# Kernel tuning notes

Hardware: AMD Instinct MI355X
Metric: run time of the kernel (lower is better)

## Reference

```python
import jax, jax.numpy as jnp
import numpy as np

XBOUND = (-30.0, 30.0, 0.25)
YBOUND = (-15.0, 15.0, 0.25)
ZBOUND = (-1.0, 1.0, 0.5)
EPS = 1e-9


def _heights():
    n = int((ZBOUND[1] - ZBOUND[0]) // ZBOUND[2]) + 1
    return [ZBOUND[0] + i * ZBOUND[2] for i in range(n)]


def _bev_planes():
    # matches construct_plane_grid: linspace endpoints included, meshgrid(y, x) 'ij'
    num_x = int((XBOUND[1] - XBOUND[0]) / XBOUND[2])
    num_y = int((YBOUND[1] - YBOUND[0]) / YBOUND[2])
    x = jnp.linspace(XBOUND[0], XBOUND[1], num_x, dtype=jnp.float32)
    y = jnp.linspace(YBOUND[0], YBOUND[1], num_y, dtype=jnp.float32)
    yy, xx = jnp.meshgrid(y, x, indexing='ij')
    planes = [jnp.stack([xx, yy, jnp.full_like(xx, h)], axis=-1) for h in _heights()]
    return jnp.stack(planes)  # (nlvl, bH, bW, 3)


def _bilinear_grid_sample(im, grid):
    # faithful port of the manual pad+floor+gather grid_sample (align_corners=False)
    n, c, h, w = im.shape
    gh, gw = grid.shape[1], grid.shape[2]
    x = ((grid[..., 0] + 1) * w - 1) / 2
    y = ((grid[..., 1] + 1) * h - 1) / 2
    x = x.reshape(n, -1)
    y = y.reshape(n, -1)
    x0 = jnp.floor(x)
    y0 = jnp.floor(y)
    wa = ((x0 + 1 - x) * (y0 + 1 - y))[:, None, :]
    wb = ((x0 + 1 - x) * (y - y0))[:, None, :]
    wc = ((x - x0) * (y0 + 1 - y))[:, None, :]
    wd = ((x - x0) * (y - y0))[:, None, :]
    pw, ph = w + 2, h + 2
    # clip in float first to avoid int32 overflow; out-of-range lands on zero padding either way
    x0f = jnp.clip(x0, -2.0, w + 2.0)
    y0f = jnp.clip(y0, -2.0, h + 2.0)
    x0i = jnp.clip(x0f.astype(jnp.int32) + 1, 0, pw - 1)
    x1i = jnp.clip(x0f.astype(jnp.int32) + 2, 0, pw - 1)
    y0i = jnp.clip(y0f.astype(jnp.int32) + 1, 0, ph - 1)
    y1i = jnp.clip(y0f.astype(jnp.int32) + 2, 0, ph - 1)
    im_flat = jnp.pad(im, ((0, 0), (0, 0), (1, 1), (1, 1))).reshape(n, c, -1)

    def gather(xi, yi):
        return jnp.take_along_axis(im_flat, (xi + yi * pw)[:, None, :], axis=2)

    out = (gather(x0i, y0i) * wa + gather(x0i, y1i) * wb
           + gather(x1i, y0i) * wc + gather(x1i, y1i) * wd)
    return out.reshape(n, c, gh, gw)


def _campos(pts, ego2cam, img_h, img_w):
    # pts: (B, q, 3); ego2cam: (B, ncam, 4, 4)
    B, q, _ = pts.shape
    ncam = ego2cam.shape[1]
    pts_h = jnp.concatenate([pts, jnp.ones_like(pts[..., :1])], axis=-1)  # (B,q,4)
    cam = jnp.einsum('bnij,bqj->bnqi', ego2cam, pts_h)  # (B,ncam,q,4)
    z = cam[..., 2:3]
    mask = z > EPS
    xy = cam[..., 0:2] / z + EPS
    px = xy[..., 0:1] / img_w
    py = xy[..., 1:2] / img_h
    p = (jnp.concatenate([px, py], axis=-1) - 0.5) * 2
    mask = (mask & (p[..., 0:1] > -1.0) & (p[..., 0:1] < 1.0)
            & (p[..., 1:2] > -1.0) & (p[..., 1:2] < 1.0))
    return p.reshape(B * ncam, q, 2), mask.reshape(B, ncam, q)


def reference(cam_feat, ego2cam, conv_w, conv_b, img_h, img_w):
    B, ncam = ego2cam.shape[0], ego2cam.shape[1]
    C = cam_feat.shape[1]
    planes = _bev_planes().astype(cam_feat.dtype)  # (nlvl,bH,bW,3)
    nlvl, bH, bW, _ = planes.shape
    pts = jnp.broadcast_to(planes.reshape(1, -1, 3), (B, nlvl * bH * bW, 3))
    pos, mask = _campos(pts, ego2cam, img_h, img_w)
    grid = pos.reshape(B * ncam, nlvl * bH, bW, 2)
    proj = _bilinear_grid_sample(cam_feat, grid).reshape(B, ncam, C, nlvl, bH, bW)
    m = mask.reshape(B, ncam, 1, nlvl, bH, bW).astype(proj.dtype)
    feat = (proj * m).sum(axis=1)            # (B,C,nlvl,bH,bW)
    num = m.sum(axis=1)                      # (B,1,nlvl,bH,bW)
    feat = feat / jnp.where(num == 0, jnp.ones_like(num), num)
    coords = jnp.broadcast_to(jnp.transpose(planes, (3, 0, 1, 2))[None], (B, 3, nlvl, bH, bW))
    feat = jnp.concatenate([feat, coords], axis=1).reshape(B, (C + 3) * nlvl, bH, bW)
    out = jax.lax.conv_general_dilated(
        feat, conv_w, window_strides=(1, 1), padding=((1, 1), (1, 1)),
        dimension_numbers=('NCHW', 'OIHW', 'NCHW'))
    return out + conv_b[None, :, None, None]


def setup_inputs() -> dict:
    key = jax.random.key(0)
    k1, k2, k3 = jax.random.split(key, 3)
    B, ncam, C = 1, 6, 128
    cH, cW = 64, 176
    nlvl = 5
    cam_feat = jax.random.normal(k1, (B * ncam, C, cH, cW), dtype=jnp.float32)
    ego2cam = jax.random.normal(k2, (B, ncam, 4, 4), dtype=jnp.float32)
    conv_w = jax.random.normal(k3, (128, (C + 3) * nlvl, 3, 3), dtype=jnp.float32) * 0.02
    conv_b = jnp.zeros((128,), dtype=jnp.float32)
    return {'cam_feat': cam_feat, 'ego2cam': ego2cam, 'conv_w': conv_w,
            'conv_b': conv_b, 'img_h': 512, 'img_w': 1408}
```

## Files before the change

kernel.cpp:

```cpp
#include <hip/hip_runtime.h>
#include <hip/hip_bf16.h>

#define BH 120
#define BW 240
#define NLVL 5
#define NCAM 6
#define CH 128
#define FH 64
#define FW 176
#define CIN 655
#define CINP 672
#define NCT 21
#define FROWS 124
#define FCOLS 242
#define NPIX (BH*BW)

typedef __hip_bfloat16 bf16;
typedef __attribute__((ext_vector_type(8))) short s16x8;
typedef __attribute__((ext_vector_type(4))) float f32x4;
typedef __attribute__((ext_vector_type(2))) float f32x2;
typedef unsigned int uint;
typedef __attribute__((ext_vector_type(4), aligned(4))) uint uint4a;

#define G_AS __attribute__((address_space(1)))
#define L_AS __attribute__((address_space(3)))

__device__ __forceinline__ float bf2f(unsigned short u) {
    union { unsigned int i; float f; } c; c.i = ((unsigned int)u) << 16; return c.f;
}
__device__ __forceinline__ uint f2bu(float x) {
    return (uint)__hip_bfloat16_raw(__float2bfloat16(x)).x;
}

__global__ __launch_bounds__(256) void transpose_kernel(
    const float* __restrict__ in, float* __restrict__ out)
{
    __shared__ float t[32][129];
    int n = blockIdx.z, h = blockIdx.y, w0 = blockIdx.x * 32;
    int wlim = min(32, FW - w0);
    int wx = threadIdx.x & 31, cg = threadIdx.x >> 5;
    if (wx < wlim) {
        #pragma unroll
        for (int k = 0; k < 16; ++k) {
            int c = cg + k * 8;
            t[wx][c] = in[((n*CH + c)*FH + h)*FW + w0 + wx];
        }
    }
    __syncthreads();
    int c2 = threadIdx.x & 127, wi = threadIdx.x >> 7;
    for (int w = wi; w < wlim; w += 2)
        out[((n*FH + h)*FW + w0 + w)*CH + c2] = t[w][c2];
}

__global__ __launch_bounds__(256) void wprep_kernel(
    const float* __restrict__ w, bf16* __restrict__ wbf)
{
    int idx = blockIdx.x * 256 + threadIdx.x;
    if (idx >= 128 * CINP) return;
    int oc = idx / CINP, cin = idx - oc * CINP;
    float v[9];
    if (cin < CIN) {
        const float* s = w + ((size_t)oc * CIN + cin) * 9;
        #pragma unroll
        for (int k = 0; k < 9; ++k) v[k] = s[k];
    } else {
        #pragma unroll
        for (int k = 0; k < 9; ++k) v[k] = 0.f;
    }
    #pragma unroll
    for (int k = 0; k < 9; ++k)
        wbf[(size_t)(k * 128 + oc) * CINP + cin] = __float2bfloat16(v[k]);
}

__global__ __launch_bounds__(128) void border_kernel(bf16* __restrict__ feat)
{
    int b = blockIdx.x;
    int row, col;
    if (b < 242)      { row = 0;   col = b; }
    else if (b < 484) { row = 121; col = b - 242; }
    else if (b < 604) { row = b - 484 + 1; col = 0; }
    else              { row = b - 604 + 1; col = 241; }
    s16x8* p = (s16x8*)(feat + ((size_t)row*FCOLS + col)*CINP);
    int t = threadIdx.x;
    if (t < 84) p[t] = (s16x8){0,0,0,0,0,0,0,0};
}

__global__ __launch_bounds__(256) void proj_kernel(
    const float* __restrict__ camt,
    const float* __restrict__ e2c,
    const int* __restrict__ pimgh, const int* __restrict__ pimgw,
    bf16* __restrict__ feat)
{
    __shared__ int   s_soff[4][32];
    __shared__ float s_w4[4][30][4];
    __shared__ int   s_val[4][32];

    const int wv = threadIdx.x >> 6;
    const int lane = threadIdx.x & 63;
    const int pix = blockIdx.x * 4 + wv;
    const int bx = pix % BW, by = pix / BW;
    float xw = (float)(-30.0 + bx * (60.0/239.0)); if (bx == BW-1) xw = 30.f;
    float yw = (float)(-15.0 + by * (30.0/119.0)); if (by == BH-1) yw = 15.f;

    const bool act = lane < 30;
    int valid = 0, ix = 0, iy = 0, cam = 0;
    float fx = 0.f, fy = 0.f;
    if (act) {
        int l = lane / 6; cam = lane - l*6;
        float h = -1.f + 0.5f * (float)l;
        const float* M = e2c + cam * 16;
        float cx = M[0]*xw + M[1]*yw + M[2]*h  + M[3];
        float cy = M[4]*xw + M[5]*yw + M[6]*h  + M[7];
        float cz = M[8]*xw + M[9]*yw + M[10]*h + M[11];
        float iw = (float)pimgw[0], ih = (float)pimgh[0];
        float px = ((cx/cz + 1e-9f)/iw - 0.5f) * 2.f;
        float py = ((cy/cz + 1e-9f)/ih - 0.5f) * 2.f;
        valid = (cz > 1e-9f) && (px > -1.f) && (px < 1.f)
                             && (py > -1.f) && (py < 1.f);
        float xs = ((px + 1.f)*(float)FW - 1.f) * 0.5f;
        float ys = ((py + 1.f)*(float)FH - 1.f) * 0.5f;
        float x0 = floorf(xs), y0 = floorf(ys);
        fx = xs - x0; fy = ys - y0;
        ix = (int)x0; iy = (int)y0;
        s_val[wv][lane] = valid;
    }
    __syncthreads();
    if (act) {
        int lbase = (lane / 6) * 6;
        int cnt = s_val[wv][lbase] + s_val[wv][lbase+1] + s_val[wv][lbase+2]
                + s_val[wv][lbase+3] + s_val[wv][lbase+4] + s_val[wv][lbase+5];
        float inv = (cnt > 0) ? (1.f / (float)cnt) : 0.f;
        float sc = valid ? inv : 0.f;
        int bx0 = min(max(ix, 0), FW-2);
        int by0 = min(max(iy, 0), FH-2);
        float gx0 = (1.f - fx) * sc, gx1 = fx * sc;
        float wx0 = 0.f, wx1 = 0.f;
        if (ix >= 0)     { if (ix == bx0) wx0 += gx0; else wx1 += gx0; }
        if (ix+1 <= FW-1){ if (ix+1 == bx0) wx0 += gx1; else wx1 += gx1; }
        float wy0 = 0.f, wy1 = 0.f;
        float gy0 = 1.f - fy, gy1 = fy;
        if (iy >= 0)     { if (iy == by0) wy0 += gy0; else wy1 += gy0; }
        if (iy+1 <= FH-1){ if (iy+1 == by0) wy0 += gy1; else wy1 += gy1; }
        s_w4[wv][lane][0] = wx0 * wy0;
        s_w4[wv][lane][1] = wx0 * wy1;
        s_w4[wv][lane][2] = wx1 * wy0;
        s_w4[wv][lane][3] = wx1 * wy1;
        s_soff[wv][lane] = valid ? ((cam*FH + by0)*FW + bx0)*CH : -1;
    }
    __syncthreads();

    const int c2 = lane * 2;
    float va[NLVL], vb[NLVL];
    #pragma unroll
    for (int l = 0; l < NLVL; ++l) { va[l] = 0.f; vb[l] = 0.f; }

    #pragma unroll
    for (int l = 0; l < NLVL; ++l) {
        #pragma unroll
        for (int cm = 0; cm < NCAM; ++cm) {
            int id = l*6 + cm;
            int so = s_soff[wv][id];
            if (so >= 0) {
                const float* bp = camt + so + c2;
                f32x2 t0 = *(const f32x2*)(bp);
                f32x2 t2 = *(const f32x2*)(bp + CH);
                f32x2 t1 = *(const f32x2*)(bp + FW*CH);
                f32x2 t3 = *(const f32x2*)(bp + FW*CH + CH);
                float w0 = s_w4[wv][id][0], w1 = s_w4[wv][id][1];
                float w2 = s_w4[wv][id][2], w3 = s_w4[wv][id][3];
                va[l] += w0*t0[0] + w1*t1[0] + w2*t2[0] + w3*t3[0];
                vb[l] += w0*t0[1] + w1*t1[1] + w2*t2[1] + w3*t3[1];
            }
        }
    }

    bf16* dpix = feat + ((size_t)(by+1)*FCOLS + (bx+1))*CINP;
    uint u0 = f2bu(va[0]) | (f2bu(va[1]) << 16);
    uint u1 = f2bu(va[2]) | (f2bu(va[3]) << 16);
    uint u2 = f2bu(va[4]) | (f2bu(vb[0]) << 16);
    uint u3 = f2bu(vb[1]) | (f2bu(vb[2]) << 16);
    uint u4 = f2bu(vb[3]) | (f2bu(vb[4]) << 16);
    char* dst = (char*)(dpix + c2*5);
    *(uint4a*)dst = (uint4a){u0, u1, u2, u3};
    *(uint*)(dst + 16) = u4;
    if (lane < 15) {
        int j = lane / 5, l = lane - j*5;
        float v = (j == 0) ? xw : (j == 1) ? yw : (-1.f + 0.5f*(float)l);
        dpix[CH*5 + lane] = __float2bfloat16(v);
    }
}

__global__ __launch_bounds__(256, 4) void conv_mfma_kernel(
    const bf16* __restrict__ feat,
    const bf16* __restrict__ wbf,
    bf16* __restrict__ part)
{
    __shared__ __align__(16) char lds[40960];
    const int tid  = threadIdx.x;
    const int wv   = tid >> 6;
    const int lane = tid & 63;
    const int t15  = tid & 15;
    const int kgl  = (tid >> 4) & 3;
    const int y0p = blockIdx.y * 8;
    const int x0p = blockIdx.x * 16;
    const int q   = blockIdx.z;
    const int ct0 = q ? (1 + 5*q) : 0;
    const int nph = (q ? 5 : 6) * 9;

    const int HB0 = 0, HB1 = 12288, WB0 = 24576, WB1 = 32768;

    f32x4 acc[8][2];
    #pragma unroll
    for (int m = 0; m < 8; ++m)
        #pragma unroll
        for (int f = 0; f < 2; ++f)
            acc[m][f] = (f32x4){0.f, 0.f, 0.f, 0.f};

    auto stageW = [&](int ct, int off, int wb) {
        #pragma unroll
        for (int jj = 0; jj < 2; ++jj) {
            int j = 2*wv + jj;
            int cch = j*64 + lane;
            int oc = cch >> 2, kgp = cch & 3;
            int kg = kgp ^ ((oc >> 1) & 3);
            const bf16* src = wbf + ((size_t)(off*128 + oc)*CINP + ct*32 + kg*8);
            __builtin_amdgcn_global_load_lds((const G_AS void*)src,
                                             (L_AS void*)(lds + wb + j*1024),
                                             16, 0, 0);
        }
    };
    auto stageH = [&](int ct, int hb) {
        #pragma unroll
        for (int kk = 0; kk < 3; ++kk) {
            int j = wv + 4*kk;
            int cch = j*64 + lane;
            int pp = cch >> 2, kgp = cch & 3;
            int kg = kgp ^ ((pp >> 1) & 3);
            int row = pp / 18;
            int col = pp - row*18;
            const bf16* src = feat + ((size_t)(y0p + row)*FCOLS + (x0p + col))*CINP
                                   + ct*32 + kg*8;
            __builtin_amdgcn_global_load_lds((const G_AS void*)src,
                                             (L_AS void*)(lds + hb + j*1024),
                                             16, 0, 0);
        }
    };

    stageH(ct0, HB0);
    stageW(ct0, 0, WB0);
    __syncthreads();

    int lct = 0, off = 0;
    for (int p = 0; p < nph; ++p) {
        if (p + 1 < nph) {
            int off1 = off + 1, lct1 = lct;
            if (off1 == 9) { off1 = 0; ++lct1; }
            stageW(ct0 + lct1, off1, ((p+1) & 1) ? WB1 : WB0);
            if (off1 == 0) stageH(ct0 + lct1, (lct1 & 1) ? HB1 : HB0);
        }
        const int wb = (p & 1) ? WB1 : WB0;
        const int hb = (lct & 1) ? HB1 : HB0;
        const int ky = off / 3, kx = off - ky*3;

        s16x8 A[8];
        #pragma unroll
        for (int m = 0; m < 8; ++m) {
            int oc = m*16 + t15;
            A[m] = *(const s16x8*)(lds + wb + oc*64 + ((kgl ^ ((oc>>1)&3)) << 4));
        }
        #pragma unroll
        for (int f = 0; f < 2; ++f) {
            int prow = (2*wv + f + ky)*18 + t15 + kx;
            s16x8 Bv = *(const s16x8*)(lds + hb + prow*64 + ((kgl ^ ((prow>>1)&3)) << 4));
            __builtin_amdgcn_s_setprio(1);
            #pragma unroll
            for (int m = 0; m < 8; ++m)
                acc[m][f] = __builtin_amdgcn_mfma_f32_16x16x32_bf16(A[m], Bv, acc[m][f], 0, 0, 0);
            __builtin_amdgcn_s_setprio(0);
        }
        __syncthreads();
        if (++off == 9) { off = 0; ++lct; }
    }

    bf16* pq = part + (size_t)q * (128*NPIX);
    const int xo = x0p + t15;
    #pragma unroll
    for (int m = 0; m < 8; ++m) {
        #pragma unroll
        for (int r = 0; r < 4; ++r) {
            int oc = m*16 + kgl*4 + r;
            #pragma unroll
            for (int f = 0; f < 2; ++f) {
                int y = y0p + 2*wv + f;
                pq[(size_t)oc*NPIX + y*BW + xo] = __float2bfloat16(acc[m][f][r]);
            }
        }
    }
}

__global__ __launch_bounds__(256) void combine_kernel(
    const bf16* __restrict__ part, const float* __restrict__ bias,
    float* __restrict__ out)
{
    int i8 = blockIdx.x * 256 + threadIdx.x;
    if (i8 >= 128*NPIX/8) return;
    int oc = i8 / (NPIX/8);
    float s[8];
    float b = bias[oc];
    #pragma unroll
    for (int k = 0; k < 8; ++k) s[k] = b;
    #pragma unroll
    for (int qq = 0; qq < 4; ++qq) {
        s16x8 v = *(const s16x8*)(part + (size_t)qq*(128*NPIX) + (size_t)i8*8);
        #pragma unroll
        for (int k = 0; k < 8; ++k) s[k] += bf2f((unsigned short)v[k]);
    }
    f32x4* o = (f32x4*)(out + (size_t)i8*8);
    o[0] = (f32x4){s[0], s[1], s[2], s[3]};
    o[1] = (f32x4){s[4], s[5], s[6], s[7]};
}

extern "C" void kernel_launch(void* const* d_in, const int* in_sizes, int n_in,
                              void* d_out, int out_size, void* d_ws, size_t ws_size,
                              hipStream_t stream)
{
    const float* cam_feat = (const float*)d_in[0];
    const float* ego2cam  = (const float*)d_in[1];
    const float* conv_w   = (const float*)d_in[2];
    const float* conv_b   = (const float*)d_in[3];
    const int*   img_h    = (const int*)d_in[4];
    const int*   img_w    = (const int*)d_in[5];
    float* out = (float*)d_out;

    float* camt = (float*)d_ws;
    bf16* feat = (bf16*)(camt + (size_t)NCAM*CH*FH*FW);
    bf16* wbf  = feat + (size_t)FROWS*FCOLS*CINP;
    bf16* part = (bf16*)d_ws;

    transpose_kernel<<<dim3(6, FH, NCAM), 256, 0, stream>>>(cam_feat, camt);
    wprep_kernel<<<(128*CINP + 255)/256, 256, 0, stream>>>(conv_w, wbf);
    border_kernel<<<724, 128, 0, stream>>>(feat);
    proj_kernel<<<NPIX/4, 256, 0, stream>>>(camt, ego2cam, img_h, img_w, feat);
    conv_mfma_kernel<<<dim3(15, 15, 4), 256, 0, stream>>>(feat, wbf, part);
    combine_kernel<<<(128*NPIX/8 + 255)/256, 256, 0, stream>>>(part, conv_b, out);
}
```

Measured before the change: 118.8 us.

## Store camera features as bf16, swizzle projection blocks, widen conv tile with register weights

Camera features are transposed into bf16 instead of fp32, which halves the gather traffic in the projection kernel. Projection blocks are remapped with a swizzle so neighbouring blocks touch different pixel rows. The conv kernel now covers 32 columns per block instead of 16, holds four accumulator fragments, and double-buffers weights in registers loaded straight from global memory instead of staging them through LDS. That cuts the block count and the barriers per kernel tap, but raises register pressure (occupancy bound lowered to 2), and sampled features lose precision.

New measurement: 168.1 us. 41.5% more time.

```diff
diff --git a/kernel.cpp b/kernel.cpp
--- a/kernel.cpp
+++ b/kernel.cpp
@@ -18,7 +18,6 @@
 typedef __hip_bfloat16 bf16;
 typedef __attribute__((ext_vector_type(8))) short s16x8;
 typedef __attribute__((ext_vector_type(4))) float f32x4;
-typedef __attribute__((ext_vector_type(2))) float f32x2;
 typedef unsigned int uint;
 typedef __attribute__((ext_vector_type(4), aligned(4))) uint uint4a;
 
@@ -31,9 +30,15 @@
 __device__ __forceinline__ uint f2bu(float x) {
     return (uint)__hip_bfloat16_raw(__float2bfloat16(x)).x;
 }
+__device__ __forceinline__ float blo(uint u) {
+    union { uint i; float f; } c; c.i = u << 16; return c.f;
+}
+__device__ __forceinline__ float bhi(uint u) {
+    union { uint i; float f; } c; c.i = u & 0xFFFF0000u; return c.f;
+}
 
 __global__ __launch_bounds__(256) void transpose_kernel(
-    const float* __restrict__ in, float* __restrict__ out)
+    const float* __restrict__ in, bf16* __restrict__ out)
 {
     __shared__ float t[32][129];
     int n = blockIdx.z, h = blockIdx.y, w0 = blockIdx.x * 32;
@@ -49,7 +54,7 @@
     __syncthreads();
     int c2 = threadIdx.x & 127, wi = threadIdx.x >> 7;
     for (int w = wi; w < wlim; w += 2)
-        out[((n*FH + h)*FW + w0 + w)*CH + c2] = t[w][c2];
+        out[((n*FH + h)*FW + w0 + w)*CH + c2] = __float2bfloat16(t[w][c2]);
 }
 
 __global__ __launch_bounds__(256) void wprep_kernel(
@@ -86,7 +91,7 @@
 }
 
 __global__ __launch_bounds__(256) void proj_kernel(
-    const float* __restrict__ camt,
+    const bf16* __restrict__ camt,
     const float* __restrict__ e2c,
     const int* __restrict__ pimgh, const int* __restrict__ pimgw,
     bf16* __restrict__ feat)
@@ -97,7 +102,9 @@
 
     const int wv = threadIdx.x >> 6;
     const int lane = threadIdx.x & 63;
-    const int pix = blockIdx.x * 4 + wv;
+    const int bid = blockIdx.x;
+    const int swz = (bid & 7) * 900 + (bid >> 3);
+    const int pix = swz * 4 + wv;
     const int bx = pix % BW, by = pix / BW;
     float xw = (float)(-30.0 + bx * (60.0/239.0)); if (bx == BW-1) xw = 30.f;
     float yw = (float)(-15.0 + by * (30.0/119.0)); if (by == BH-1) yw = 15.f;
@@ -161,15 +168,15 @@
             int id = l*6 + cm;
             int so = s_soff[wv][id];
             if (so >= 0) {
-                const float* bp = camt + so + c2;
-                f32x2 t0 = *(const f32x2*)(bp);
-                f32x2 t2 = *(const f32x2*)(bp + CH);
-                f32x2 t1 = *(const f32x2*)(bp + FW*CH);
-                f32x2 t3 = *(const f32x2*)(bp + FW*CH + CH);
+                const bf16* bp = camt + so + c2;
+                uint q0 = *(const uint*)(bp);
+                uint q2 = *(const uint*)(bp + CH);
+                uint q1 = *(const uint*)(bp + FW*CH);
+                uint q3 = *(const uint*)(bp + FW*CH + CH);
                 float w0 = s_w4[wv][id][0], w1 = s_w4[wv][id][1];
                 float w2 = s_w4[wv][id][2], w3 = s_w4[wv][id][3];
-                va[l] += w0*t0[0] + w1*t1[0] + w2*t2[0] + w3*t3[0];
-                vb[l] += w0*t0[1] + w1*t1[1] + w2*t2[1] + w3*t3[1];
+                va[l] += w0*blo(q0) + w1*blo(q1) + w2*blo(q2) + w3*blo(q3);
+                vb[l] += w0*bhi(q0) + w1*bhi(q1) + w2*bhi(q2) + w3*bhi(q3);
             }
         }
     }
@@ -190,109 +197,104 @@
     }
 }
 
-__global__ __launch_bounds__(256, 4) void conv_mfma_kernel(
+__global__ __launch_bounds__(256, 2) void conv_mfma_kernel(
     const bf16* __restrict__ feat,
     const bf16* __restrict__ wbf,
     bf16* __restrict__ part)
 {
-    __shared__ __align__(16) char lds[40960];
+    __shared__ __align__(16) char lds[45056];
     const int tid  = threadIdx.x;
     const int wv   = tid >> 6;
     const int lane = tid & 63;
     const int t15  = tid & 15;
     const int kgl  = (tid >> 4) & 3;
     const int y0p = blockIdx.y * 8;
-    const int x0p = blockIdx.x * 16;
+    const int x0p = blockIdx.x * 32;
     const int q   = blockIdx.z;
     const int ct0 = q ? (1 + 5*q) : 0;
-    const int nph = (q ? 5 : 6) * 9;
-
-    const int HB0 = 0, HB1 = 12288, WB0 = 24576, WB1 = 32768;
-
-    f32x4 acc[8][2];
+    const int nct = q ? 5 : 6;
+    const int HBS = 22528;
+
+    f32x4 acc[8][4];
     #pragma unroll
     for (int m = 0; m < 8; ++m)
         #pragma unroll
-        for (int f = 0; f < 2; ++f)
+        for (int f = 0; f < 4; ++f)
             acc[m][f] = (f32x4){0.f, 0.f, 0.f, 0.f};
 
-    auto stageW = [&](int ct, int off, int wb) {
-        #pragma unroll
-        for (int jj = 0; jj < 2; ++jj) {
-            int j = 2*wv + jj;
-            int cch = j*64 + lane;
-            int oc = cch >> 2, kgp = cch & 3;
-            int kg = kgp ^ ((oc >> 1) & 3);
-            const bf16* src = wbf + ((size_t)(off*128 + oc)*CINP + ct*32 + kg*8);
-            __builtin_amdgcn_global_load_lds((const G_AS void*)src,
-                                             (L_AS void*)(lds + wb + j*1024),
-                                             16, 0, 0);
-        }
-    };
     auto stageH = [&](int ct, int hb) {
-        #pragma unroll
-        for (int kk = 0; kk < 3; ++kk) {
-            int j = wv + 4*kk;
+        for (int j = wv; j < 22; j += 4) {
             int cch = j*64 + lane;
             int pp = cch >> 2, kgp = cch & 3;
             int kg = kgp ^ ((pp >> 1) & 3);
-            int row = pp / 18;
-            int col = pp - row*18;
-            const bf16* src = feat + ((size_t)(y0p + row)*FCOLS + (x0p + col))*CINP
+            int row = pp / 34;
+            int col = pp - row*34;
+            int gc = min(x0p + col, FCOLS-1);
+            const bf16* src = feat + ((size_t)(y0p + row)*FCOLS + gc)*CINP
                                    + ct*32 + kg*8;
             __builtin_amdgcn_global_load_lds((const G_AS void*)src,
                                              (L_AS void*)(lds + hb + j*1024),
                                              16, 0, 0);
         }
     };
-
-    stageH(ct0, HB0);
-    stageW(ct0, 0, WB0);
+    auto loadA = [&](int ct, int off, s16x8* A) {
+        const bf16* base = wbf + ((size_t)(off*128 + t15))*CINP + ct*32 + kgl*8;
+        #pragma unroll
+        for (int m = 0; m < 8; ++m)
+            A[m] = *(const s16x8*)(base + (size_t)m*16*CINP);
+    };
+
+    s16x8 A0[8], A1[8];
+    stageH(ct0, 0);
+    loadA(ct0, 0, A0);
     __syncthreads();
 
-    int lct = 0, off = 0;
-    for (int p = 0; p < nph; ++p) {
-        if (p + 1 < nph) {
-            int off1 = off + 1, lct1 = lct;
-            if (off1 == 9) { off1 = 0; ++lct1; }
-            stageW(ct0 + lct1, off1, ((p+1) & 1) ? WB1 : WB0);
-            if (off1 == 0) stageH(ct0 + lct1, (lct1 & 1) ? HB1 : HB0);
-        }
-        const int wb = (p & 1) ? WB1 : WB0;
-        const int hb = (lct & 1) ? HB1 : HB0;
-        const int ky = off / 3, kx = off - ky*3;
-
-        s16x8 A[8];
-        #pragma unroll
-        for (int m = 0; m < 8; ++m) {
-            int oc = m*16 + t15;
-            A[m] = *(const s16x8*)(lds + wb + oc*64 + ((kgl ^ ((oc>>1)&3)) << 4));
-        }
-        #pragma unroll
-        for (int f = 0; f < 2; ++f) {
-            int prow = (2*wv + f + ky)*18 + t15 + kx;
-            s16x8 Bv = *(const s16x8*)(lds + hb + prow*64 + ((kgl ^ ((prow>>1)&3)) << 4));
-            __builtin_amdgcn_s_setprio(1);
+    for (int c = 0; c < nct; ++c) {
+        const int ct = ct0 + c;
+        const int hb = (c & 1) ? HBS : 0;
+        if (c + 1 < nct) stageH(ct + 1, (c & 1) ? 0 : HBS);
+        #pragma unroll
+        for (int off = 0; off < 9; ++off) {
+            s16x8* Au = (off & 1) ? A1 : A0;
+            s16x8* Al = (off & 1) ? A0 : A1;
+            if (off < 8)            loadA(ct, off + 1, Al);
+            else if (c + 1 < nct)   loadA(ct + 1, 0, Al);
+            const int ky = off / 3, kx = off - ky*3;
             #pragma unroll
-            for (int m = 0; m < 8; ++m)
-                acc[m][f] = __builtin_amdgcn_mfma_f32_16x16x32_bf16(A[m], Bv, acc[m][f], 0, 0, 0);
-            __builtin_amdgcn_s_setprio(0);
+            for (int f = 0; f < 4; ++f) {
+                const int fr = f >> 1, fc = f & 1;
+                int hp = (2*wv + fr + ky)*34 + fc*16 + t15 + kx;
+                s16x8 Bv = *(const s16x8*)(lds + hb + hp*64
+                                           + ((kgl ^ ((hp>>1)&3)) << 4));
+                __builtin_amdgcn_s_setprio(1);
+                #pragma unroll
+                for (int m = 0; m < 8; ++m)
+                    acc[m][f] = __builtin_amdgcn_mfma_f32_16x16x32_bf16(
+                                    Au[m], Bv, acc[m][f], 0, 0, 0);
+                __builtin_amdgcn_s_setprio(0);
+            }
+        }
+        if (c + 1 < nct) {
+            #pragma unroll
+            for (int m = 0; m < 8; ++m) A0[m] = A1[m];
         }
         __syncthreads();
-        if (++off == 9) { off = 0; ++lct; }
     }
 
     bf16* pq = part + (size_t)q * (128*NPIX);
-    const int xo = x0p + t15;
-    #pragma unroll
-    for (int m = 0; m < 8; ++m) {
-        #pragma unroll
-        for (int r = 0; r < 4; ++r) {
-            int oc = m*16 + kgl*4 + r;
+    #pragma unroll
+    for (int f = 0; f < 4; ++f) {
+        const int fr = f >> 1, fc = f & 1;
+        const int x = x0p + fc*16 + t15;
+        if (x < BW) {
+            const int y = y0p + 2*wv + fr;
             #pragma unroll
-            for (int f = 0; f < 2; ++f) {
-                int y = y0p + 2*wv + f;
-                pq[(size_t)oc*NPIX + y*BW + xo] = __float2bfloat16(acc[m][f][r]);
+            for (int m = 0; m < 8; ++m) {
+                #pragma unroll
+                for (int r = 0; r < 4; ++r) {
+                    int oc = m*16 + kgl*4 + r;
+                    pq[(size_t)oc*NPIX + y*BW + x] = __float2bfloat16(acc[m][f][r]);
+                }
             }
         }
     }
@@ -332,15 +334,15 @@
     const int*   img_w    = (const int*)d_in[5];
     float* out = (float*)d_out;
 
-    float* camt = (float*)d_ws;
-    bf16* feat = (bf16*)(camt + (size_t)NCAM*CH*FH*FW);
+    bf16* camt = (bf16*)d_ws;
+    bf16* feat = camt + (size_t)NCAM*CH*FH*FW;
     bf16* wbf  = feat + (size_t)FROWS*FCOLS*CINP;
-    bf16* part = (bf16*)d_ws;
+    bf16* part = wbf  + (size_t)9*128*CINP;
 
     transpose_kernel<<<dim3(6, FH, NCAM), 256, 0, stream>>>(cam_feat, camt);
     wprep_kernel<<<(128*CINP + 255)/256, 256, 0, stream>>>(conv_w, wbf);
     border_kernel<<<724, 128, 0, stream>>>(feat);
     proj_kernel<<<NPIX/4, 256, 0, stream>>>(camt, ego2cam, img_h, img_w, feat);
-    conv_mfma_kernel<<<dim3(15, 15, 4), 256, 0, stream>>>(feat, wbf, part);
+    conv_mfma_kernel<<<dim3(8, 15, 4), 256, 0, stream>>>(feat, wbf, part);
     combine_kernel<<<(128*NPIX/8 + 255)/256, 256, 0, stream>>>(part, conv_b, out);
 }
```
